# Optimization experiments

Measured on AMD Instinct MI355X. Metric: run time of the kernel, lower is better.

Reference implementation:

```python
import jax, jax.numpy as jnp
import numpy as np

DIM = 256
NUM_LAYERS = 6
STRENGTHS = jnp.array([0.1, 0.1, 0.05], dtype=jnp.float32)  # entail, contra, neutral
MAX_NORM = 10.0
EPS = 1e-8          # ops.eps()
NORM_EPS = 1e-12    # F.normalize eps
B = 131072


def _normalize(x, axis=-1):
    # matches torch F.normalize(p=2): x / max(||x||, 1e-12)
    n = jnp.linalg.norm(x, axis=axis, keepdims=True)
    return x / jnp.maximum(n, NORM_EPS)


def setup_inputs() -> dict:
    key = jax.random.key(0)
    ks = jax.random.split(key, 6)
    return {
        "h0": jax.random.normal(ks[0], (B, DIM), dtype=jnp.float32),
        "W1": jax.random.normal(ks[1], (DIM, DIM), dtype=jnp.float32) * 0.05,
        "b1": jax.random.normal(ks[2], (DIM,), dtype=jnp.float32) * 0.05,
        "W2": jax.random.normal(ks[3], (DIM, DIM), dtype=jnp.float32) * 0.05,
        "b2": jax.random.normal(ks[4], (DIM,), dtype=jnp.float32) * 0.05,
        "anchors": jax.random.normal(ks[5], (3, DIM), dtype=jnp.float32),
    }


def reference(h0, W1, b1, W2, b2, anchors):
    anchors_n = _normalize(anchors, axis=-1)  # [3, D], normalized once before the loop

    def step(h, _):
        h_n = _normalize(h)                              # [B, D]
        # physics: alignment = cos sim, divergence = 1 - alignment, tension = div^2
        align = h_n @ anchors_n.T                        # [B, 3]
        div = 1.0 - align                                # [B, 3]
        tens = div * div                                 # [B, 3] (traced, not fed back)
        # anchor forces: -strength * div * normalize(h - anchor)
        direction = _normalize(h[:, None, :] - anchors_n[None, :, :])   # [B, 3, D]
        total_force = jnp.einsum('bk,bkd->bd', -(STRENGTHS[None, :] * div), direction)
        # 2-layer MLP update
        delta = jnp.tanh(h @ W1.T + b1) @ W2.T + b2      # [B, D]
        h_new = h + delta + total_force
        # norm clipping
        n = jnp.linalg.norm(h_new, axis=-1, keepdims=True)
        h_new = jnp.where(n > MAX_NORM, h_new * (MAX_NORM / (n + EPS)), h_new)
        return h_new, (align, div, tens)

    h_final, (aligns, divs, tens) = jax.lax.scan(step, h0, None, length=NUM_LAYERS)
    # aligns/divs/tens: [L, B, 3] traces, axis -1 = (entail, contra, neutral)
    return h_final, aligns, divs, tens
```

## Files before the change

### kernel.cpp

```cpp
#include <hip/hip_runtime.h>
#include <math.h>


#define DIMX 256
#define NL 6
#define CPAD 68

typedef float f32x4 __attribute__((ext_vector_type(4)));
typedef short short8 __attribute__((ext_vector_type(8)));
typedef unsigned int u32x4 __attribute__((ext_vector_type(4)));

#define CHB(c) ((c) * 1024)
#define EXTB 16384

#define PACKB(X0, X1, DST)                                                       \
    asm("v_cvt_pk_bf16_f32 %0, %1, %2" : "=v"(DST) : "v"(X0), "v"(X1));

__global__ void wsplit(const float* __restrict__ W1, const float* __restrict__ W2,
                       const float* __restrict__ anchors, const float* __restrict__ b2f,
                       u32x4* __restrict__ ws) {
    int gi = blockIdx.x * 256 + threadIdx.x;
    if (gi < 16384) {
        int ln   = gi & 63;
        int t8   = (gi >> 6) & 7;
        int ks2  = (gi >> 9) & 1;
        int kk   = (gi >> 10) & 3;
        int pass = (gi >> 12) & 1;
        int g    = (gi >> 13) & 1;
        int ks   = kk * 2 + ks2;
        int m    = (pass * 8 + t8) * 16 + (ln & 15);
        int G    = ln >> 4;
        const float* Wg = g ? W2 : W1;
        unsigned o[4];
#pragma unroll
        for (int p = 0; p < 4; ++p) {
            int f = 32 * ks + ((p >> 1) << 4) + 4 * G + ((p & 1) << 1);
            float x0 = Wg[m * DIMX + f];
            float x1 = Wg[m * DIMX + f + 1];
            unsigned hp;
            PACKB(x0, x1, hp);
            o[p] = hp;
        }
        u32x4 out = {o[0], o[1], o[2], o[3]};
        ws[gi] = out;
    } else {
        int r    = gi - EXTB;
        int pass = r >> 9;
        int t8   = (r >> 6) & 7;
        int ln   = r & 63;
        int m    = ln & 15;
        int G    = ln >> 4;
        int fout = (pass * 8 + t8) * 16 + m;
        float inv[3];
#pragma unroll
        for (int k = 0; k < 3; ++k) {
            float ss = 0.0f;
            for (int f = 0; f < DIMX; ++f) {
                float a = anchors[k * DIMX + f];
                ss += a * a;
            }
            inv[k] = 1.0f / fmaxf(sqrtf(ss), 1e-12f);
        }
        float v[8];
#pragma unroll
        for (int i = 0; i < 8; ++i) {
            int k = G * 8 + i;
            v[i] = (k == 0) ? -anchors[fout] * inv[0]
                 : (k == 1) ? -anchors[DIMX + fout] * inv[1]
                 : (k == 2) ? -anchors[2 * DIMX + fout] * inv[2]
                 : (k == 3) ? b2f[fout] : 0.0f;
        }
        unsigned o[4];
#pragma unroll
        for (int p = 0; p < 4; ++p) {
            unsigned hp;
            PACKB(v[2 * p], v[2 * p + 1], hp);
            o[p] = hp;
        }
        u32x4 out = {o[0], o[1], o[2], o[3]};
        ws[gi] = out;
    }
}


#define STAGE(gIdxBase, ldsSlotBase)                                             \
    {                                                                            \
        _Pragma("unroll")                                                        \
        for (int i_ = 0; i_ < 2; ++i_) {                                         \
            const int off_ = ((w * 2 + i_) << 6);                                \
            __builtin_amdgcn_global_load_lds(                                    \
                (const __attribute__((address_space(1))) void*)(ws + (gIdxBase) + off_ + lane), \
                (__attribute__((address_space(3))) void*)(&wf[(ldsSlotBase) + off_]),           \
                16, 0, 0);                                                       \
        }                                                                        \
    }

#define PIPE_SYNC()                                                              \
    {                                                                            \
        asm volatile("s_waitcnt vmcnt(4)" ::: "memory");                         \
        __builtin_amdgcn_sched_barrier(0);                                       \
        __builtin_amdgcn_s_barrier();                                            \
        __builtin_amdgcn_sched_barrier(0);                                       \
    }

__global__ __launch_bounds__(512, 2)
void collapse_mfma16(const float* __restrict__ h0,
                     const float* __restrict__ b1f,
                     const float* __restrict__ anchors,
                     const u32x4* __restrict__ ws,
                     float* __restrict__ out_h,
                     float* __restrict__ out_align,
                     float* __restrict__ out_div,
                     float* __restrict__ out_tens,
                     int B)
{
    __shared__ __align__(16) u32x4 wf[4096];
    __shared__ __align__(16) u32x4 wext[1024];
    __shared__ __align__(16) float an_reg[3][272];
    __shared__ __align__(16) float b1_reg[272];
    __shared__ float an_inv[3];

    const int tid  = threadIdx.x;
    const int w    = tid >> 6;
    const int lane = tid & 63;
    const int G    = lane >> 4;
    const int c    = lane & 15;
    const int bglob = blockIdx.x * 128 + w * 16 + c;

    {
#pragma unroll
        for (int i_ = 0; i_ < 2; ++i_) {
            const int off_ = ((w * 2 + i_) << 6);
            __builtin_amdgcn_global_load_lds(
                (const __attribute__((address_space(1))) void*)(ws + EXTB + off_ + lane),
                (__attribute__((address_space(3))) void*)(&wext[off_]),
                16, 0, 0);
        }
    }

    if (w < 3) {
        const float4 av = *(const float4*)&anchors[w * DIMX + lane * 4];
        float ss = av.x * av.x + av.y * av.y + av.z * av.z + av.w * av.w;
#pragma unroll
        for (int m = 1; m < 64; m <<= 1) ss += __shfl_xor(ss, m, 64);
        if (lane == 0) an_inv[w] = 1.0f / fmaxf(sqrtf(ss), 1e-12f);
    }
    __syncthreads();

    {
        int idx = tid & 255;
        int Gc = idx >> 6, s = idx & 63;
        int f = 16 * (s >> 2) + 4 * Gc + (s & 3);
        int pidx = Gc * CPAD + s;
        if (tid < 256) {
            b1_reg[pidx] = b1f[f];
        } else {
#pragma unroll
            for (int k = 0; k < 3; ++k)
                an_reg[k][pidx] = anchors[k * DIMX + f] * an_inv[k];
        }
    }
    __syncthreads();

    float hr[64];
#pragma unroll
    for (int mt = 0; mt < 16; ++mt) {
        const float4 v = *(const float4*)&h0[(size_t)bglob * DIMX + 16 * mt + 4 * G];
        hr[mt * 4 + 0] = v.x; hr[mt * 4 + 1] = v.y;
        hr[mt * 4 + 2] = v.z; hr[mt * 4 + 3] = v.w;
    }

    STAGE(CHB(0), 0);
    STAGE(CHB(1), 1024);
    STAGE(CHB(2), 2048);

#pragma unroll 1
    for (int layer = 0; layer < NL; ++layer) {
        float p0 = 0, d0 = 0, d1 = 0, d2 = 0;
#pragma unroll
        for (int q = 0; q < 16; ++q) {
            const float4 a0 = *(const float4*)&an_reg[0][G * CPAD + q * 4];
            const float4 a1 = *(const float4*)&an_reg[1][G * CPAD + q * 4];
            const float4 a2 = *(const float4*)&an_reg[2][G * CPAD + q * 4];
            float x;
            x = hr[q*4+0]; p0 += x*x; d0 += x*a0.x; d1 += x*a1.x; d2 += x*a2.x;
            x = hr[q*4+1]; p0 += x*x; d0 += x*a0.y; d1 += x*a1.y; d2 += x*a2.y;
            x = hr[q*4+2]; p0 += x*x; d0 += x*a0.z; d1 += x*a1.z; d2 += x*a2.z;
            x = hr[q*4+3]; p0 += x*x; d0 += x*a0.w; d1 += x*a1.w; d2 += x*a2.w;
        }
        p0 += __shfl_xor(p0, 16); d0 += __shfl_xor(d0, 16);
        d1 += __shfl_xor(d1, 16); d2 += __shfl_xor(d2, 16);
        p0 += __shfl_xor(p0, 32); d0 += __shfl_xor(d0, 32);
        d1 += __shfl_xor(d1, 32); d2 += __shfl_xor(d2, 32);
        const float inv_rn = 1.0f / fmaxf(sqrtf(p0), 1e-12f);
        const float al0 = d0 * inv_rn, al1 = d1 * inv_rn, al2 = d2 * inv_rn;
        const float dv0 = 1.0f - al0, dv1 = 1.0f - al1, dv2 = 1.0f - al2;
        const float c0 = -0.10f * dv0 / fmaxf(sqrtf(fmaxf(p0 - 2.0f*d0 + 1.0f, 0.0f)), 1e-12f);
        const float c1 = -0.10f * dv1 / fmaxf(sqrtf(fmaxf(p0 - 2.0f*d1 + 1.0f, 0.0f)), 1e-12f);
        const float c2 = -0.05f * dv2 / fmaxf(sqrtf(fmaxf(p0 - 2.0f*d2 + 1.0f, 0.0f)), 1e-12f);
        if (G == 0) {
            const long long tb = ((long long)layer * B + bglob) * 3;
            out_align[tb+0] = al0; out_align[tb+1] = al1; out_align[tb+2] = al2;
            out_div[tb+0] = dv0;   out_div[tb+1] = dv1;   out_div[tb+2] = dv2;
            out_tens[tb+0] = dv0*dv0; out_tens[tb+1] = dv1*dv1; out_tens[tb+2] = dv2*dv2;
        }
        unsigned be0 = 0, be1 = 0;
        if (G == 0) {
            PACKB(c0, c1, be0);
            PACKB(c2, 1.0f, be1);
        }
        u32x4 bev = {be0, be1, 0u, 0u};
        const short8 Bext = __builtin_bit_cast(short8, bev);

        unsigned tph[32];
#pragma unroll
        for (int pass = 0; pass < 2; ++pass) {
            f32x4 ac[8];
#pragma unroll
            for (int j = 0; j < 8; ++j) ac[j] = (f32x4)(0.0f);
#pragma unroll
            for (int kk = 0; kk < 4; ++kk) {
                const int s = pass * 4 + kk;
                PIPE_SYNC();
                STAGE(CHB((s + 3) & 15), ((s + 3) & 3) * 1024);
                const int cb = (s & 3) * 1024;
#pragma unroll
                for (int ks2 = 0; ks2 < 2; ++ks2) {
                    const int ks = kk * 2 + ks2;
                    unsigned bh[4];
#pragma unroll
                    for (int p = 0; p < 4; ++p)
                        PACKB(hr[8*ks + 2*p], hr[8*ks + 2*p + 1], bh[p]);
                    u32x4 thi = {bh[0], bh[1], bh[2], bh[3]};
                    const short8 Bh = __builtin_bit_cast(short8, thi);
#pragma unroll
                    for (int j = 0; j < 8; ++j) {
                        const short8 Ah = __builtin_bit_cast(short8,
                            wf[cb + ks2*512 + j*64 + lane]);
                        ac[j] = __builtin_amdgcn_mfma_f32_16x16x32_bf16(Ah, Bh, ac[j], 0, 0, 0);
                    }
                }
            }
#pragma unroll
            for (int j = 0; j < 8; ++j) {
                const int mt = pass * 8 + j;
                const float4 bq = *(const float4*)&b1_reg[G * CPAD + mt * 4];
                float tv[4];
#pragma unroll
                for (int r = 0; r < 4; ++r) {
                    float x = ac[j][r] + ((r==0)?bq.x:(r==1)?bq.y:(r==2)?bq.z:bq.w);
                    float e = __expf(2.0f * x);
                    tv[r] = 1.0f - 2.0f * __builtin_amdgcn_rcpf(e + 1.0f);
                }
                const int ti = 4 * (mt >> 1) + 2 * (mt & 1);
                PACKB(tv[0], tv[1], tph[ti]);
                PACKB(tv[2], tv[3], tph[ti + 1]);
            }
        }

        const float csum = 1.0f + c0 + c1 + c2;
#pragma unroll
        for (int pass = 0; pass < 2; ++pass) {
            f32x4 ac[8];
#pragma unroll
            for (int j = 0; j < 8; ++j) {
                const int mt = pass * 8 + j;
                ac[j][0] = hr[mt*4+0]*csum;
                ac[j][1] = hr[mt*4+1]*csum;
                ac[j][2] = hr[mt*4+2]*csum;
                ac[j][3] = hr[mt*4+3]*csum;
            }
#pragma unroll
            for (int j = 0; j < 8; ++j) {
                const short8 Ax = __builtin_bit_cast(short8, wext[pass*512 + j*64 + lane]);
                ac[j] = __builtin_amdgcn_mfma_f32_16x16x32_bf16(Ax, Bext, ac[j], 0, 0, 0);
            }
#pragma unroll
            for (int kk = 0; kk < 4; ++kk) {
                const int s = 8 + pass * 4 + kk;
                PIPE_SYNC();
                STAGE(CHB((s + 3) & 15), ((s + 3) & 3) * 1024);
                const int cb = (s & 3) * 1024;
#pragma unroll
                for (int ks2 = 0; ks2 < 2; ++ks2) {
                    const int ks = kk * 2 + ks2;
                    u32x4 thi = {tph[4*ks+0], tph[4*ks+1], tph[4*ks+2], tph[4*ks+3]};
                    const short8 Bh = __builtin_bit_cast(short8, thi);
#pragma unroll
                    for (int j = 0; j < 8; ++j) {
                        const short8 Ah = __builtin_bit_cast(short8,
                            wf[cb + ks2*512 + j*64 + lane]);
                        ac[j] = __builtin_amdgcn_mfma_f32_16x16x32_bf16(Ah, Bh, ac[j], 0, 0, 0);
                    }
                }
            }
#pragma unroll
            for (int j = 0; j < 8; ++j) {
                const int mt = pass * 8 + j;
                hr[mt*4+0] = ac[j][0]; hr[mt*4+1] = ac[j][1];
                hr[mt*4+2] = ac[j][2]; hr[mt*4+3] = ac[j][3];
            }
        }

        {
            float ss = 0.0f;
#pragma unroll
            for (int s = 0; s < 64; ++s) ss += hr[s] * hr[s];
            ss += __shfl_xor(ss, 16);
            ss += __shfl_xor(ss, 32);
            const float n = sqrtf(ss);
            const float sc = (n > 10.0f) ? (10.0f / (n + 1e-8f)) : 1.0f;
#pragma unroll
            for (int s = 0; s < 64; ++s) hr[s] *= sc;
        }
    }

#pragma unroll
    for (int mt = 0; mt < 16; ++mt) {
        float4 v;
        v.x = hr[mt*4+0]; v.y = hr[mt*4+1]; v.z = hr[mt*4+2]; v.w = hr[mt*4+3];
        *(float4*)&out_h[(size_t)bglob * DIMX + 16 * mt + 4 * G] = v;
    }
}

extern "C" void kernel_launch(void* const* d_in, const int* in_sizes, int n_in,
                              void* d_out, int out_size, void* d_ws, size_t ws_size,
                              hipStream_t stream) {
    const float* h0      = (const float*)d_in[0];
    const float* W1      = (const float*)d_in[1];
    const float* b1      = (const float*)d_in[2];
    const float* W2      = (const float*)d_in[3];
    const float* b2      = (const float*)d_in[4];
    const float* anchors = (const float*)d_in[5];
    const int B = in_sizes[0] / DIMX;

    float* out_h     = (float*)d_out;
    float* out_align = out_h + (long long)B * DIMX;
    float* out_div   = out_align + (long long)NL * B * 3;
    float* out_tens  = out_div   + (long long)NL * B * 3;

    u32x4* ws = (u32x4*)d_ws;

    hipLaunchKernelGGL(wsplit, dim3(68), dim3(256), 0, stream, W1, W2, anchors, b2, ws);
    hipLaunchKernelGGL(collapse_mfma16, dim3(B / 128), dim3(512), 0, stream,
                       h0, b1, anchors, ws,
                       out_h, out_align, out_div, out_tens, B);
}
```

Before: 333.1 us.

## Compute anchor dot products with MFMA fused into first MLP GEMM

Moves the per-row anchor dot products out of scalar FMA loops over LDS and into an extra bf16 MFMA per k-step, using a pre-packed normalized-anchor matrix built by the weight-prep kernel. The alignment computation is reordered after the first GEMM, and the anchor normalization and LDS staging in the main kernel are removed. This cuts VALU and LDS traffic per layer, but the alignment and divergence outputs now come from bf16-rounded h and anchors, which lowers precision. It also adds a shuffle to broadcast csum, since the MFMA output layout places results only in certain lanes.

```diff
diff --git a/kernel.cpp b/kernel.cpp
--- a/kernel.cpp
+++ b/kernel.cpp
@@ -12,6 +12,7 @@
 
 #define CHB(c) ((c) * 1024)
 #define EXTB 16384
+#define STATB 17408
 
 #define PACKB(X0, X1, DST)                                                       \
     asm("v_cvt_pk_bf16_f32 %0, %1, %2" : "=v"(DST) : "v"(X0), "v"(X1));
@@ -43,7 +44,7 @@
         }
         u32x4 out = {o[0], o[1], o[2], o[3]};
         ws[gi] = out;
-    } else {
+    } else if (gi < STATB) {
         int r    = gi - EXTB;
         int pass = r >> 9;
         int t8   = (r >> 6) & 7;
@@ -55,10 +56,7 @@
 #pragma unroll
         for (int k = 0; k < 3; ++k) {
             float ss = 0.0f;
-            for (int f = 0; f < DIMX; ++f) {
-                float a = anchors[k * DIMX + f];
-                ss += a * a;
-            }
+            for (int f = 0; f < DIMX; ++f) { float a = anchors[k*DIMX+f]; ss += a*a; }
             inv[k] = 1.0f / fmaxf(sqrtf(ss), 1e-12f);
         }
         float v[8];
@@ -72,11 +70,30 @@
         }
         unsigned o[4];
 #pragma unroll
-        for (int p = 0; p < 4; ++p) {
-            unsigned hp;
-            PACKB(v[2 * p], v[2 * p + 1], hp);
-            o[p] = hp;
-        }
+        for (int p = 0; p < 4; ++p) { unsigned hp; PACKB(v[2*p], v[2*p+1], hp); o[p] = hp; }
+        u32x4 out = {o[0], o[1], o[2], o[3]};
+        ws[gi] = out;
+    } else if (gi < STATB + 512) {
+        int r  = gi - STATB;
+        int ks = r >> 6;
+        int ln = r & 63;
+        int m  = ln & 15;
+        int G  = ln >> 4;
+        float inv = 0.0f;
+        if (m < 3) {
+            float ss = 0.0f;
+            for (int f = 0; f < DIMX; ++f) { float a = anchors[m*DIMX+f]; ss += a*a; }
+            inv = 1.0f / fmaxf(sqrtf(ss), 1e-12f);
+        }
+        float v[8];
+#pragma unroll
+        for (int i = 0; i < 8; ++i) {
+            int f = 32 * ks + 16 * (i >> 2) + 4 * G + (i & 3);
+            v[i] = (m < 3) ? anchors[m * DIMX + f] * inv : 0.0f;
+        }
+        unsigned o[4];
+#pragma unroll
+        for (int p = 0; p < 4; ++p) { unsigned hp; PACKB(v[2*p], v[2*p+1], hp); o[p] = hp; }
         u32x4 out = {o[0], o[1], o[2], o[3]};
         ws[gi] = out;
     }
@@ -106,7 +123,6 @@
 __global__ __launch_bounds__(512, 2)
 void collapse_mfma16(const float* __restrict__ h0,
                      const float* __restrict__ b1f,
-                     const float* __restrict__ anchors,
                      const u32x4* __restrict__ ws,
                      float* __restrict__ out_h,
                      float* __restrict__ out_align,
@@ -116,9 +132,8 @@
 {
     __shared__ __align__(16) u32x4 wf[4096];
     __shared__ __align__(16) u32x4 wext[1024];
-    __shared__ __align__(16) float an_reg[3][272];
+    __shared__ __align__(16) u32x4 wstat[512];
     __shared__ __align__(16) float b1_reg[272];
-    __shared__ float an_inv[3];
 
     const int tid  = threadIdx.x;
     const int w    = tid >> 6;
@@ -136,29 +151,17 @@
                 (__attribute__((address_space(3))) void*)(&wext[off_]),
                 16, 0, 0);
         }
-    }
-
-    if (w < 3) {
-        const float4 av = *(const float4*)&anchors[w * DIMX + lane * 4];
-        float ss = av.x * av.x + av.y * av.y + av.z * av.z + av.w * av.w;
-#pragma unroll
-        for (int m = 1; m < 64; m <<= 1) ss += __shfl_xor(ss, m, 64);
-        if (lane == 0) an_inv[w] = 1.0f / fmaxf(sqrtf(ss), 1e-12f);
-    }
-    __syncthreads();
+        __builtin_amdgcn_global_load_lds(
+            (const __attribute__((address_space(1))) void*)(ws + STATB + w*64 + lane),
+            (__attribute__((address_space(3))) void*)(&wstat[w*64]),
+            16, 0, 0);
+    }
 
     {
         int idx = tid & 255;
         int Gc = idx >> 6, s = idx & 63;
         int f = 16 * (s >> 2) + 4 * Gc + (s & 3);
-        int pidx = Gc * CPAD + s;
-        if (tid < 256) {
-            b1_reg[pidx] = b1f[f];
-        } else {
-#pragma unroll
-            for (int k = 0; k < 3; ++k)
-                an_reg[k][pidx] = anchors[k * DIMX + f] * an_inv[k];
-        }
+        if (tid < 256) b1_reg[Gc * CPAD + s] = b1f[f];
     }
     __syncthreads();
 
@@ -176,22 +179,64 @@
 
 #pragma unroll 1
     for (int layer = 0; layer < NL; ++layer) {
-        float p0 = 0, d0 = 0, d1 = 0, d2 = 0;
-#pragma unroll
-        for (int q = 0; q < 16; ++q) {
-            const float4 a0 = *(const float4*)&an_reg[0][G * CPAD + q * 4];
-            const float4 a1 = *(const float4*)&an_reg[1][G * CPAD + q * 4];
-            const float4 a2 = *(const float4*)&an_reg[2][G * CPAD + q * 4];
-            float x;
-            x = hr[q*4+0]; p0 += x*x; d0 += x*a0.x; d1 += x*a1.x; d2 += x*a2.x;
-            x = hr[q*4+1]; p0 += x*x; d0 += x*a0.y; d1 += x*a1.y; d2 += x*a2.y;
-            x = hr[q*4+2]; p0 += x*x; d0 += x*a0.z; d1 += x*a1.z; d2 += x*a2.z;
-            x = hr[q*4+3]; p0 += x*x; d0 += x*a0.w; d1 += x*a1.w; d2 += x*a2.w;
-        }
-        p0 += __shfl_xor(p0, 16); d0 += __shfl_xor(d0, 16);
-        d1 += __shfl_xor(d1, 16); d2 += __shfl_xor(d2, 16);
-        p0 += __shfl_xor(p0, 32); d0 += __shfl_xor(d0, 32);
-        d1 += __shfl_xor(d1, 32); d2 += __shfl_xor(d2, 32);
+        float p0 = 0;
+#pragma unroll
+        for (int s = 0; s < 64; ++s) p0 += hr[s] * hr[s];
+        p0 += __shfl_xor(p0, 16);
+        p0 += __shfl_xor(p0, 32);
+
+        unsigned tph[32];
+        f32x4 acs = (f32x4)(0.0f);
+#pragma unroll
+        for (int pass = 0; pass < 2; ++pass) {
+            f32x4 ac[8];
+#pragma unroll
+            for (int j = 0; j < 8; ++j) ac[j] = (f32x4)(0.0f);
+#pragma unroll
+            for (int kk = 0; kk < 4; ++kk) {
+                const int s = pass * 4 + kk;
+                PIPE_SYNC();
+                STAGE(CHB((s + 3) & 15), ((s + 3) & 3) * 1024);
+                const int cb = (s & 3) * 1024;
+#pragma unroll
+                for (int ks2 = 0; ks2 < 2; ++ks2) {
+                    const int ks = kk * 2 + ks2;
+                    unsigned bh[4];
+#pragma unroll
+                    for (int p = 0; p < 4; ++p)
+                        PACKB(hr[8*ks + 2*p], hr[8*ks + 2*p + 1], bh[p]);
+                    u32x4 thi = {bh[0], bh[1], bh[2], bh[3]};
+                    const short8 Bh = __builtin_bit_cast(short8, thi);
+#pragma unroll
+                    for (int j = 0; j < 8; ++j) {
+                        const short8 Ah = __builtin_bit_cast(short8,
+                            wf[cb + ks2*512 + j*64 + lane]);
+                        ac[j] = __builtin_amdgcn_mfma_f32_16x16x32_bf16(Ah, Bh, ac[j], 0, 0, 0);
+                    }
+                    if (pass == 0) {
+                        const short8 As = __builtin_bit_cast(short8, wstat[ks*64 + lane]);
+                        acs = __builtin_amdgcn_mfma_f32_16x16x32_bf16(As, Bh, acs, 0, 0, 0);
+                    }
+                }
+            }
+#pragma unroll
+            for (int j = 0; j < 8; ++j) {
+                const int mt = pass * 8 + j;
+                const float4 bq = *(const float4*)&b1_reg[G * CPAD + mt * 4];
+                float tv[4];
+#pragma unroll
+                for (int r = 0; r < 4; ++r) {
+                    float x = ac[j][r] + ((r==0)?bq.x:(r==1)?bq.y:(r==2)?bq.z:bq.w);
+                    float e = __expf(2.0f * x);
+                    tv[r] = 1.0f - 2.0f * __builtin_amdgcn_rcpf(e + 1.0f);
+                }
+                const int ti = 4 * (mt >> 1) + 2 * (mt & 1);
+                PACKB(tv[0], tv[1], tph[ti]);
+                PACKB(tv[2], tv[3], tph[ti + 1]);
+            }
+        }
+
+        const float d0 = acs[0], d1 = acs[1], d2 = acs[2];
         const float inv_rn = 1.0f / fmaxf(sqrtf(p0), 1e-12f);
         const float al0 = d0 * inv_rn, al1 = d1 * inv_rn, al2 = d2 * inv_rn;
         const float dv0 = 1.0f - al0, dv1 = 1.0f - al1, dv2 = 1.0f - al2;
@@ -205,60 +250,12 @@
             out_tens[tb+0] = dv0*dv0; out_tens[tb+1] = dv1*dv1; out_tens[tb+2] = dv2*dv2;
         }
         unsigned be0 = 0, be1 = 0;
-        if (G == 0) {
-            PACKB(c0, c1, be0);
-            PACKB(c2, 1.0f, be1);
-        }
+        if (G == 0) { PACKB(c0, c1, be0); PACKB(c2, 1.0f, be1); }
         u32x4 bev = {be0, be1, 0u, 0u};
         const short8 Bext = __builtin_bit_cast(short8, bev);
-
-        unsigned tph[32];
-#pragma unroll
-        for (int pass = 0; pass < 2; ++pass) {
-            f32x4 ac[8];
-#pragma unroll
-            for (int j = 0; j < 8; ++j) ac[j] = (f32x4)(0.0f);
-#pragma unroll
-            for (int kk = 0; kk < 4; ++kk) {
-                const int s = pass * 4 + kk;
-                PIPE_SYNC();
-                STAGE(CHB((s + 3) & 15), ((s + 3) & 3) * 1024);
-                const int cb = (s & 3) * 1024;
-#pragma unroll
-                for (int ks2 = 0; ks2 < 2; ++ks2) {
-                    const int ks = kk * 2 + ks2;
-                    unsigned bh[4];
-#pragma unroll
-                    for (int p = 0; p < 4; ++p)
-                        PACKB(hr[8*ks + 2*p], hr[8*ks + 2*p + 1], bh[p]);
-                    u32x4 thi = {bh[0], bh[1], bh[2], bh[3]};
-                    const short8 Bh = __builtin_bit_cast(short8, thi);
-#pragma unroll
-                    for (int j = 0; j < 8; ++j) {
-                        const short8 Ah = __builtin_bit_cast(short8,
-                            wf[cb + ks2*512 + j*64 + lane]);
-                        ac[j] = __builtin_amdgcn_mfma_f32_16x16x32_bf16(Ah, Bh, ac[j], 0, 0, 0);
-                    }
-                }
-            }
-#pragma unroll
-            for (int j = 0; j < 8; ++j) {
-                const int mt = pass * 8 + j;
-                const float4 bq = *(const float4*)&b1_reg[G * CPAD + mt * 4];
-                float tv[4];
-#pragma unroll
-                for (int r = 0; r < 4; ++r) {
-                    float x = ac[j][r] + ((r==0)?bq.x:(r==1)?bq.y:(r==2)?bq.z:bq.w);
-                    float e = __expf(2.0f * x);
-                    tv[r] = 1.0f - 2.0f * __builtin_amdgcn_rcpf(e + 1.0f);
-                }
-                const int ti = 4 * (mt >> 1) + 2 * (mt & 1);
-                PACKB(tv[0], tv[1], tph[ti]);
-                PACKB(tv[2], tv[3], tph[ti + 1]);
-            }
-        }
-
-        const float csum = 1.0f + c0 + c1 + c2;
+        float csum = 1.0f + c0 + c1 + c2;
+        csum = __shfl(csum, c);
+
 #pragma unroll
         for (int pass = 0; pass < 2; ++pass) {
             f32x4 ac[8];
@@ -341,8 +338,8 @@
 
     u32x4* ws = (u32x4*)d_ws;
 
-    hipLaunchKernelGGL(wsplit, dim3(68), dim3(256), 0, stream, W1, W2, anchors, b2, ws);
+    hipLaunchKernelGGL(wsplit, dim3(70), dim3(256), 0, stream, W1, W2, anchors, b2, ws);
     hipLaunchKernelGGL(collapse_mfma16, dim3(B / 128), dim3(512), 0, stream,
-                       h0, b1, anchors, ws,
+                       h0, b1, ws,
                        out_h, out_align, out_div, out_tens, B);
 }
```

Result: no change. 337.0 us (+1.2%).
